# Kernel optimization log

Measured on AMD Instinct MI355X. Metric: run time of the kernel, lower is better.

## Reference

```python
import jax, jax.numpy as jnp
import numpy as np

B, P = 8, 1024
D = 512
BUCKETS = 65536
LS = (8, 7, 6)  # padded ids per patch for ngrams 1,2,3


def setup_inputs() -> dict:
    key = jax.random.key(0)
    ks = jax.random.split(key, 10)
    inp = {}
    for i, L in enumerate(LS):
        inp[f"ids_{i+1}"] = jax.random.randint(ks[i], (B, P, L), 0, BUCKETS, dtype=jnp.int64)
        inp[f"mask_{i+1}"] = jax.random.randint(ks[3 + i], (B, P, L), 0, 2, dtype=jnp.int32).astype(bool)
        inp[f"emb_{i+1}"] = jax.random.normal(ks[6 + i], (BUCKETS, D), dtype=jnp.float32)
    inp["patch_mask"] = jax.random.randint(ks[9], (B, P), 0, 2, dtype=jnp.int32).astype(bool)
    return inp


def reference(ids_1, ids_2, ids_3, mask_1, mask_2, mask_3, patch_mask, emb_1, emb_2, emb_3):
    # For each ngram order: gather [B,P,L,D], zero out padded ids, sum over L.
    out = jnp.zeros((B, P, D), dtype=emb_1.dtype)
    for ids, m, emb in ((ids_1, mask_1, emb_1), (ids_2, mask_2, emb_2), (ids_3, mask_3, emb_3)):
        g = jnp.take(emb, ids, axis=0)               # [B,P,L,D]
        out = out + jnp.where(m[..., None], g, 0).sum(axis=2)
    return jnp.where(patch_mask[..., None], out, 0)
```

## Files before the change

kernel.cpp:

```cpp
#include <hip/hip_runtime.h>


#define D_DIM 512
#define NPATCH 8192

__device__ __forceinline__ void acc_add(float4& a, const float4 b) {
    a.x += b.x; a.y += b.y; a.z += b.z; a.w += b.w;
}

template <int L>
__device__ __forceinline__ void gather_sum(const int* __restrict__ ids,
                                           const int* __restrict__ mask,
                                           const float* __restrict__ emb,
                                           int lane, float4& acc0, float4& acc1) {
#pragma unroll
    for (int l = 0; l < L; ++l) {
        if (mask[l]) {
            const float4* row = (const float4*)(emb + (size_t)ids[l] * D_DIM);
            acc_add(acc0, row[lane]);
            acc_add(acc1, row[64 + lane]);
        }
    }
}

__global__ __launch_bounds__(256) void patch_embed_kernel(
    const int* __restrict__ ids1, const int* __restrict__ m1, const float* __restrict__ e1,
    const int* __restrict__ ids2, const int* __restrict__ m2, const float* __restrict__ e2,
    const int* __restrict__ ids3, const int* __restrict__ m3, const float* __restrict__ e3,
    const int* __restrict__ pmask, float* __restrict__ out) {
    const int wave  = threadIdx.x >> 6;
    const int lane  = threadIdx.x & 63;
    const int patch = (blockIdx.x << 2) | wave;

    float4 acc0 = make_float4(0.f, 0.f, 0.f, 0.f);
    float4 acc1 = make_float4(0.f, 0.f, 0.f, 0.f);

    if (pmask[patch]) {
        gather_sum<8>(ids1 + patch * 8, m1 + patch * 8, e1, lane, acc0, acc1);
        gather_sum<7>(ids2 + patch * 7, m2 + patch * 7, e2, lane, acc0, acc1);
        gather_sum<6>(ids3 + patch * 6, m3 + patch * 6, e3, lane, acc0, acc1);
    }

    float4* outv = (float4*)(out + (size_t)patch * D_DIM);
    outv[lane]      = acc0;
    outv[64 + lane] = acc1;
}

extern "C" void kernel_launch(void* const* d_in, const int* in_sizes, int n_in,
                              void* d_out, int out_size, void* d_ws, size_t ws_size,
                              hipStream_t stream) {
    const int*   ids1  = (const int*)d_in[0];
    const int*   m1    = (const int*)d_in[1];
    const float* e1    = (const float*)d_in[2];
    const int*   ids2  = (const int*)d_in[3];
    const int*   m2    = (const int*)d_in[4];
    const float* e2    = (const float*)d_in[5];
    const int*   ids3  = (const int*)d_in[6];
    const int*   m3    = (const int*)d_in[7];
    const float* e3    = (const float*)d_in[8];
    const int*   pmask = (const int*)d_in[9];
    float* out = (float*)d_out;

    dim3 grid(NPATCH / 4);
    dim3 block(256);
    patch_embed_kernel<<<grid, block, 0, stream>>>(ids1, m1, e1, ids2, m2, e2,
                                                   ids3, m3, e3, pmask, out);
}
```

Baseline: 311.3 us.

## Split each patch across two waves and issue all row loads before summing

Each wave now handles half of a patch's 512-wide row, doubling the grid to 16384 waves. All up to 21 masked row loads go into separate registers and are summed afterwards, instead of accumulating after each load. This lets many independent loads be in flight at once to hide gather latency. Mask and id values are made wave-uniform with readfirstlane so the branches and addresses are scalar. The cost is higher register use per thread, 21 float4 temporaries, which may lower occupancy.

```diff
diff --git a/kernel.cpp b/kernel.cpp
--- a/kernel.cpp
+++ b/kernel.cpp
@@ -1,24 +1,24 @@
 #include <hip/hip_runtime.h>
 
 
-#define D_DIM 512
-#define NPATCH 8192
+#define D_DIM   512
+#define NPATCH  8192
+#define NWAVES  (NPATCH * 2)
 
 __device__ __forceinline__ void acc_add(float4& a, const float4 b) {
     a.x += b.x; a.y += b.y; a.z += b.z; a.w += b.w;
 }
 
 template <int L>
-__device__ __forceinline__ void gather_sum(const int* __restrict__ ids,
-                                           const int* __restrict__ mask,
-                                           const float* __restrict__ emb,
-                                           int lane, float4& acc0, float4& acc1) {
+__device__ __forceinline__ void gather_stage(const int* __restrict__ ids,
+                                             const int* __restrict__ mask,
+                                             const float* __restrict__ emb,
+                                             int foff, float4* __restrict__ t) {
 #pragma unroll
     for (int l = 0; l < L; ++l) {
-        if (mask[l]) {
-            const float4* row = (const float4*)(emb + (size_t)ids[l] * D_DIM);
-            acc_add(acc0, row[lane]);
-            acc_add(acc1, row[64 + lane]);
+        if (__builtin_amdgcn_readfirstlane(mask[l])) {
+            const int sid = __builtin_amdgcn_readfirstlane(ids[l]);
+            t[l] = *(const float4*)(emb + (size_t)sid * D_DIM + foff);
         }
     }
 }
@@ -28,22 +28,26 @@
     const int* __restrict__ ids2, const int* __restrict__ m2, const float* __restrict__ e2,
     const int* __restrict__ ids3, const int* __restrict__ m3, const float* __restrict__ e3,
     const int* __restrict__ pmask, float* __restrict__ out) {
-    const int wave  = threadIdx.x >> 6;
-    const int lane  = threadIdx.x & 63;
-    const int patch = (blockIdx.x << 2) | wave;
+    const int lane = threadIdx.x & 63;
+    const int gw   = (blockIdx.x << 2) | (threadIdx.x >> 6);
+    const int patch = __builtin_amdgcn_readfirstlane(gw >> 1);
+    const int foff  = ((gw & 1) << 8) | (lane << 2);
 
-    float4 acc0 = make_float4(0.f, 0.f, 0.f, 0.f);
-    float4 acc1 = make_float4(0.f, 0.f, 0.f, 0.f);
+    float4 t[21];
+#pragma unroll
+    for (int i = 0; i < 21; ++i) t[i] = make_float4(0.f, 0.f, 0.f, 0.f);
 
-    if (pmask[patch]) {
-        gather_sum<8>(ids1 + patch * 8, m1 + patch * 8, e1, lane, acc0, acc1);
-        gather_sum<7>(ids2 + patch * 7, m2 + patch * 7, e2, lane, acc0, acc1);
-        gather_sum<6>(ids3 + patch * 6, m3 + patch * 6, e3, lane, acc0, acc1);
+    if (__builtin_amdgcn_readfirstlane(pmask[patch])) {
+        gather_stage<8>(ids1 + patch * 8, m1 + patch * 8, e1, foff, t);
+        gather_stage<7>(ids2 + patch * 7, m2 + patch * 7, e2, foff, t + 8);
+        gather_stage<6>(ids3 + patch * 6, m3 + patch * 6, e3, foff, t + 15);
     }
 
-    float4* outv = (float4*)(out + (size_t)patch * D_DIM);
-    outv[lane]      = acc0;
-    outv[64 + lane] = acc1;
+    float4 acc = t[0];
+#pragma unroll
+    for (int i = 1; i < 21; ++i) acc_add(acc, t[i]);
+
+    *(float4*)(out + (size_t)patch * D_DIM + foff) = acc;
 }
 
 extern "C" void kernel_launch(void* const* d_in, const int* in_sizes, int n_in,
@@ -61,7 +65,7 @@
     const int*   pmask = (const int*)d_in[9];
     float* out = (float*)d_out;
 
-    dim3 grid(NPATCH / 4);
+    dim3 grid(NWAVES / 4);
     dim3 block(256);
     patch_embed_kernel<<<grid, block, 0, stream>>>(ids1, m1, e1, ids2, m2, e2,
                                                    ids3, m3, e3, pmask, out);
```

After: 307.2 us. About the same (-1.3%).
